# Optimization experiments

Hardware: AMD Instinct MI355X
Metric: run time of the kernel (lower is better)

The kernel has to match this reference:

```python
import jax, jax.numpy as jnp
import numpy as np

NUM_CLASSES = 21
THRESH = 0.5
VAR = (0.1, 0.2)
B, P, O = 128, 8732, 16

def setup_inputs() -> dict:
    key = jax.random.key(0)
    ks = jax.random.split(key, 7)
    loc_preds = jax.random.normal(ks[0], (B, P, 4), jnp.float32)
    score_preds = jax.random.normal(ks[1], (B, P, NUM_CLASSES), jnp.float32)
    # priors in center-size form (cx, cy, w, h)
    pc = jax.random.uniform(ks[2], (P, 2), minval=0.05, maxval=0.95)
    pwh = jax.random.uniform(ks[3], (P, 2), minval=0.05, maxval=0.4)
    priors = jnp.concatenate([pc, pwh], axis=1).astype(jnp.float32)
    # ground truth: valid point-form boxes + label in last column
    gc = jax.random.uniform(ks[4], (B, O, 2), minval=0.2, maxval=0.8)
    gwh = jax.random.uniform(ks[5], (B, O, 2), minval=0.05, maxval=0.3)
    boxes = jnp.concatenate([gc - gwh / 2, gc + gwh / 2], axis=-1)
    labels = jax.random.randint(ks[6], (B, O, 1), 1, NUM_CLASSES).astype(jnp.float32)
    gt_data = jnp.concatenate([boxes, labels], axis=-1).astype(jnp.float32)
    return {"loc_preds": loc_preds, "score_preds": score_preds,
            "gt_data": gt_data, "priors": priors}

def _iou(a, b):
    # a: (O,4) point form, b: (P,4) point form -> (O,P)
    lt = jnp.maximum(a[:, None, :2], b[None, :, :2])
    rb = jnp.minimum(a[:, None, 2:], b[None, :, 2:])
    wh = jnp.clip(rb - lt, 0.0)
    inter = wh[..., 0] * wh[..., 1]
    area_a = (a[:, 2] - a[:, 0]) * (a[:, 3] - a[:, 1])
    area_b = (b[:, 2] - b[:, 0]) * (b[:, 3] - b[:, 1])
    return inter / (area_a[:, None] + area_b[None, :] - inter)

def _encode(matched, priors):
    # matched: (P,4) point form; priors: (P,4) center-size form
    g_c = (matched[:, :2] + matched[:, 2:]) / 2 - priors[:, :2]
    g_c = g_c / (VAR[0] * priors[:, 2:])
    g_wh = (matched[:, 2:] - matched[:, :2]) / priors[:, 2:]
    g_wh = jnp.log(g_wh) / VAR[1]
    return jnp.concatenate([g_c, g_wh], axis=1)

def _match_one(gt_loc, gt_cls, priors_pt, priors):
    ious = _iou(gt_loc, priors_pt)                    # (O, P)
    best_prior_idx = jnp.argmax(ious, axis=1)         # (O,)
    best_truth_overlap = jnp.max(ious, axis=0)        # (P,)
    best_truth_idx = jnp.argmax(ious, axis=0)         # (P,)
    # ensure every gt's best prior is kept positive and assigned to that gt
    best_truth_overlap = best_truth_overlap.at[best_prior_idx].set(2.0)
    best_truth_idx = best_truth_idx.at[best_prior_idx].set(jnp.arange(gt_loc.shape[0]))
    matched = gt_loc[best_truth_idx]                  # (P, 4)
    conf = gt_cls[best_truth_idx]
    conf = jnp.where(best_truth_overlap < THRESH, 0.0, conf)
    return _encode(matched, priors), conf.astype(jnp.int32)

def reference(loc_preds, score_preds, gt_data, priors):
    priors_pt = jnp.concatenate([priors[:, :2] - priors[:, 2:] / 2,
                                 priors[:, :2] + priors[:, 2:] / 2], axis=1)
    gt_loc, gt_cls = gt_data[..., :4], gt_data[..., 4]
    loc_targets, score_targets = jax.vmap(
        lambda l, c: _match_one(l, c, priors_pt, priors))(gt_loc, gt_cls)
    pos = score_targets > 0                           # (B, P)
    num_matched = jnp.sum(pos).astype(jnp.float32)

    # SmoothL1 over positive boxes (sum reduction)
    d = jnp.abs(loc_preds - loc_targets)
    sl1 = jnp.where(d < 1.0, 0.5 * d * d, d - 0.5)    # (B, P, 4)
    loc_loss = jnp.sum(jnp.where(pos[..., None], sl1, 0.0))

    # per-box cross-entropy on all boxes
    lse = jax.nn.logsumexp(score_preds, axis=-1)      # (B, P)
    gathered = jnp.take_along_axis(score_preds, score_targets[..., None],
                                   axis=-1)[..., 0]
    ce = lse - gathered                               # (B, P)

    # hard negative mining via double argsort ranking
    mine = jnp.where(pos, 0.0, ce)
    idx = jnp.argsort(-mine, axis=1)
    rank = jnp.argsort(idx, axis=1)
    num_pos = jnp.sum(pos, axis=1)                    # (B,)
    total_pos = jnp.sum(num_pos)
    num_neg = jnp.minimum(3 * num_pos, P - total_pos - 1)
    neg = rank < num_neg[:, None]

    sel = pos | neg
    conf_loss = jnp.sum(jnp.where(sel, ce, 0.0))
    return loc_loss / num_matched, conf_loss / num_matched
```

## Files before the change

### kernel.cpp

```cpp
#include <hip/hip_runtime.h>
#include <cstdint>
#include <cstddef>

#define B 128
#define P 8732
#define NC 21
#define O 16
#define THRESH 0.5f
#define NB1 8
#define NBX2 6
#define BPB 1456
#define WPW 364
#define NPART (B * NBX2)
#define SLABF 1536

typedef unsigned long long u64;
typedef unsigned int u32;
typedef unsigned char u8;

__device__ __forceinline__ float iou_pt(float a0, float a1, float a2, float a3,
                                        float b0, float b1, float b2, float b3) {
    float ltx = fmaxf(a0, b0), lty = fmaxf(a1, b1);
    float rbx = fminf(a2, b2), rby = fminf(a3, b3);
    float wx = fmaxf(rbx - ltx, 0.0f), wy = fmaxf(rby - lty, 0.0f);
    float inter = wx * wy;
    float aa = (a2 - a0) * (a3 - a1);
    float ab = (b2 - b0) * (b3 - b1);
    return inter / (aa + ab - inter);
}

__global__ void __launch_bounds__(256) k_pass1(const float* __restrict__ gt,
                                               const float* __restrict__ priors,
                                               u64* __restrict__ bk,
                                               u8* __restrict__ bidx) {
    const int b = blockIdx.y;
    __shared__ float s_gt[O * 4];
    __shared__ u64 s_wk[4][O];
    const int tid = threadIdx.x;
    const int wave = tid >> 6, lane = tid & 63;
    if (tid < O * 4) {
        int o = tid >> 2, c = tid & 3;
        s_gt[tid] = gt[(b * O + o) * 5 + c];
    }
    __syncthreads();

    u64 lk[O];
#pragma unroll
    for (int o = 0; o < O; o++) lk[o] = 0ull;

    for (int p = blockIdx.x * 256 + tid; p < P; p += NB1 * 256) {
        float4 pr = reinterpret_cast<const float4*>(priors)[p];
        float b0 = pr.x - pr.z * 0.5f, b1 = pr.y - pr.w * 0.5f;
        float b2 = pr.x + pr.z * 0.5f, b3 = pr.y + pr.w * 0.5f;
        float bov = -1.0f; int bo = 0;
#pragma unroll
        for (int o = 0; o < O; o++) {
            float v = iou_pt(s_gt[o * 4 + 0], s_gt[o * 4 + 1], s_gt[o * 4 + 2], s_gt[o * 4 + 3],
                             b0, b1, b2, b3);
            u64 key = ((u64)__float_as_uint(v) << 32) | (u64)(0xFFFFFFFFu - (u32)p);
            lk[o] = (key > lk[o]) ? key : lk[o];
            if (v > bov) { bov = v; bo = o; }
        }
        bidx[(size_t)b * P + p] = (u8)(bo | ((bov >= THRESH) ? 0x80 : 0));
    }

#pragma unroll
    for (int o = 0; o < O; o++) {
        u64 k = lk[o];
#pragma unroll
        for (int off = 32; off > 0; off >>= 1) {
            u64 other = (u64)__shfl_xor((long long)k, off, 64);
            k = (other > k) ? other : k;
        }
        if (lane == 0) s_wk[wave][o] = k;
    }
    __syncthreads();
    if (tid < O) {
        u64 k = s_wk[0][tid];
#pragma unroll
        for (int w = 1; w < 4; w++) { u64 v = s_wk[w][tid]; k = (v > k) ? v : k; }
        bk[((size_t)b * O + tid) * NB1 + blockIdx.x] = k;
    }
}

__device__ __forceinline__ void stage64(const float* __restrict__ gsrc,
                                        float* lds, int nf4, int lane) {
    const char* src = (const char*)gsrc;
    char* dst = (char*)lds;
#pragma unroll
    for (int i = 0; i < 6; i++) {
        int idx = i * 64 + lane;
        if (idx >= nf4) idx = nf4 - 1;
        __builtin_amdgcn_global_load_lds(
            (const __attribute__((address_space(1))) u32*)(src + (size_t)idx * 16),
            (__attribute__((address_space(3))) u32*)(dst + i * 1024),
            16, 0, 0);
    }
}

__global__ void __launch_bounds__(256) k_pass2(const float* __restrict__ gt,
                                               const float* __restrict__ priors,
                                               const u64* __restrict__ bk,
                                               const u8* __restrict__ bidx,
                                               const float* __restrict__ loc_preds,
                                               const float* __restrict__ scores,
                                               float* __restrict__ mine,
                                               double* __restrict__ pl,
                                               double* __restrict__ pc,
                                               int* __restrict__ pn) {
    const int b = blockIdx.y;
    const int tid = threadIdx.x;
    const int wave = tid >> 6, lane = tid & 63;
    __shared__ float s_slab[4][2][SLABF];
    __shared__ float s_gt[O * 5];
    __shared__ int s_bp[O];

    if (tid < O * 5) s_gt[tid] = gt[b * O * 5 + tid];
    if (tid < O) {
        u64 k = bk[((size_t)b * O + tid) * NB1];
#pragma unroll
        for (int i = 1; i < NB1; i++) {
            u64 v = bk[((size_t)b * O + tid) * NB1 + i];
            k = (v > k) ? v : k;
        }
        s_bp[tid] = (int)(0xFFFFFFFFu - (u32)(k & 0xFFFFFFFFull));
    }
    __syncthreads();

    const int wbase = blockIdx.x * BPB + wave * WPW;
    int wp = P - wbase; if (wp > WPW) wp = WPW;
    const int nchunk = (wp > 0) ? ((wp + 63) >> 6) : 0;

    double l_loc = 0.0, l_ce = 0.0;
    int l_np = 0;

    if (nchunk > 0) {
        {
            int nv0 = wp < 64 ? wp : 64;
            stage64(scores + ((size_t)b * P + wbase) * NC,
                    &s_slab[wave][0][0], nv0 * 21 / 4, lane);
        }
        for (int c = 0; c < nchunk; ++c) {
            const int base = wbase + c * 64;
            int nv = wp - c * 64; if (nv > 64) nv = 64;

            if (c + 1 < nchunk) {
                int nv2 = wp - (c + 1) * 64; if (nv2 > 64) nv2 = 64;
                asm volatile("s_waitcnt lgkmcnt(0)" ::: "memory");
                stage64(scores + ((size_t)b * P + base + 64) * NC,
                        &s_slab[wave][(c + 1) & 1][0], nv2 * 21 / 4, lane);
                asm volatile("s_waitcnt vmcnt(6)" ::: "memory");
            } else {
                asm volatile("s_waitcnt vmcnt(0)" ::: "memory");
            }
            __builtin_amdgcn_sched_barrier(0);

            if (lane < nv) {
                const int p = base + lane;
                const float* fsl = &s_slab[wave][c & 1][lane * NC];
                float fs[NC];
#pragma unroll
                for (int cc = 0; cc < NC; cc++) fs[cc] = fsl[cc];

                int e = (int)bidx[(size_t)b * P + p];
                int best_idx = e & 0x3F;
                bool matched = (e & 0x80) != 0;
#pragma unroll
                for (int o = 0; o < O; o++) {
                    if (s_bp[o] == p) { best_idx = o; matched = true; }
                }
                int cls = matched ? (int)s_gt[best_idx * 5 + 4] : 0;

                float mx = fs[0];
#pragma unroll
                for (int cc = 1; cc < NC; cc++) mx = fmaxf(mx, fs[cc]);
                float se = 0.0f;
#pragma unroll
                for (int cc = 0; cc < NC; cc++) se += __expf(fs[cc] - mx);
                float lse = mx + __logf(se);
                float g = fs[0];
#pragma unroll
                for (int cc = 1; cc < NC; cc++) g = (cc == cls) ? fs[cc] : g;
                float ce = lse - g;

                bool pos = cls > 0;
                mine[(size_t)b * P + p] = pos ? 0.0f : ce;

                if (pos) {
                    l_np++;
                    l_ce += (double)ce;
                    float4 pr = reinterpret_cast<const float4*>(priors)[p];
                    float m0 = s_gt[best_idx * 5 + 0], m1 = s_gt[best_idx * 5 + 1];
                    float m2 = s_gt[best_idx * 5 + 2], m3 = s_gt[best_idx * 5 + 3];
                    float tx = ((m0 + m2) * 0.5f - pr.x) / (0.1f * pr.z);
                    float ty = ((m1 + m3) * 0.5f - pr.y) / (0.1f * pr.w);
                    float tw = __logf((m2 - m0) / pr.z) * 5.0f;
                    float th = __logf((m3 - m1) / pr.w) * 5.0f;
                    float4 lp = reinterpret_cast<const float4*>(loc_preds)[(size_t)b * P + p];
                    float d0 = fabsf(lp.x - tx), d1 = fabsf(lp.y - ty);
                    float d2 = fabsf(lp.z - tw), d3 = fabsf(lp.w - th);
                    float s0 = d0 < 1.0f ? 0.5f * d0 * d0 : d0 - 0.5f;
                    float s1 = d1 < 1.0f ? 0.5f * d1 * d1 : d1 - 0.5f;
                    float s2 = d2 < 1.0f ? 0.5f * d2 * d2 : d2 - 0.5f;
                    float s3 = d3 < 1.0f ? 0.5f * d3 * d3 : d3 - 0.5f;
                    l_loc += (double)((s0 + s1) + (s2 + s3));
                }
            }
        }
    }

#pragma unroll
    for (int off = 32; off > 0; off >>= 1) {
        l_loc += __shfl_xor(l_loc, off, 64);
        l_ce  += __shfl_xor(l_ce, off, 64);
        l_np  += __shfl_xor(l_np, off, 64);
    }
    __shared__ double s_loc[4], s_ce[4];
    __shared__ int s_np[4];
    if (lane == 0) { s_loc[wave] = l_loc; s_ce[wave] = l_ce; s_np[wave] = l_np; }
    __syncthreads();
    if (tid == 0) {
        int q = b * NBX2 + blockIdx.x;
        pl[q] = (s_loc[0] + s_loc[1]) + (s_loc[2] + s_loc[3]);
        pc[q] = (s_ce[0] + s_ce[1]) + (s_ce[2] + s_ce[3]);
        pn[q] = s_np[0] + s_np[1] + s_np[2] + s_np[3];
    }
}

__global__ void __launch_bounds__(1024) k_hardneg(const float* __restrict__ mine,
                                                  const int* __restrict__ pn,
                                                  double* __restrict__ pneg) {
    const int b = blockIdx.x;
    const int tid = threadIdx.x;
    const int lane = tid & 63, wave = tid >> 6;
    __shared__ float s_mine[P];
    __shared__ u32 s_hist[256];
    __shared__ u32 s_sel[2];
    __shared__ double s_red[16];
    __shared__ int s_ti[16];
    __shared__ int s_npx[NBX2];
    __shared__ int s_k;

    {
        int t = 0;
        for (int i = tid; i < NPART; i += 1024) t += pn[i];
#pragma unroll
        for (int off = 32; off > 0; off >>= 1) t += __shfl_xor(t, off, 64);
        if (lane == 0) s_ti[wave] = t;
    }
    if (tid < NBX2) s_npx[tid] = pn[b * NBX2 + tid];
    __syncthreads();
    if (tid == 0) {
        int tp = 0;
#pragma unroll
        for (int w = 0; w < 16; w++) tp += s_ti[w];
        int np = 0;
#pragma unroll
        for (int x = 0; x < NBX2; x++) np += s_npx[x];
        int k = 3 * np;
        int cap = P - tp - 1;
        if (cap < k) k = cap;
        s_k = k;
    }
    __syncthreads();
    const int k = s_k;

    if (k <= 0) {
        if (tid == 0) pneg[b] = 0.0;
        return;
    }

    for (int i = tid; i < P; i += 1024) s_mine[i] = mine[(size_t)b * P + i];
    if (tid == 0) { s_sel[0] = 0u; s_sel[1] = (u32)k; }
    __syncthreads();

    for (int shift = 24; shift >= 0; shift -= 8) {
        if (tid < 256) s_hist[tid] = 0u;
        __syncthreads();
        u32 prefix = s_sel[0];
        u32 kr = s_sel[1];
        u32 himask = (shift == 24) ? 0u : (0xFFFFFFFFu << (shift + 8));
        for (int i = tid; i < P; i += 1024) {
            u32 v = __float_as_uint(s_mine[i]);
            if ((v & himask) == prefix) atomicAdd(&s_hist[(v >> shift) & 255u], 1u);
        }
        __syncthreads();
        if (tid < 64) {
            const int L = tid;
            const int btop = 255 - 4 * L;
            u32 h0 = s_hist[btop], h1 = s_hist[btop - 1], h2 = s_hist[btop - 2], h3 = s_hist[btop - 3];
            u32 g4 = h0 + h1 + h2 + h3;
            u32 x = g4;
#pragma unroll
            for (int off = 1; off < 64; off <<= 1) {
                u32 v = __shfl_up(x, off, 64);
                if (L >= off) x += v;
            }
            u32 excl = x - g4;
            if (excl < kr && excl + g4 >= kr) {
                u32 c = excl; int chosen = btop; u32 kloc = kr;
                u32 nc;
                nc = c + h0; if (c < kr && nc >= kr) { chosen = btop;     kloc = kr - c; } c = nc;
                nc = c + h1; if (c < kr && nc >= kr) { chosen = btop - 1; kloc = kr - c; } c = nc;
                nc = c + h2; if (c < kr && nc >= kr) { chosen = btop - 2; kloc = kr - c; } c = nc;
                nc = c + h3; if (c < kr && nc >= kr) { chosen = btop - 3; kloc = kr - c; } c = nc;
                s_sel[0] = prefix | ((u32)chosen << shift);
                s_sel[1] = kloc;
            }
        }
        __syncthreads();
    }

    u32 tbits = s_sel[0];
    u32 kr = s_sel[1];
    float T = __uint_as_float(tbits);

    double sd = 0.0;
    for (int i = tid; i < P; i += 1024) {
        u32 v = __float_as_uint(s_mine[i]);
        if (v > tbits) sd += (double)s_mine[i];
    }
#pragma unroll
    for (int off = 32; off > 0; off >>= 1) sd += __shfl_xor(sd, off, 64);
    if (lane == 0) s_red[wave] = sd;
    __syncthreads();
    if (tid == 0) {
        double tt = 0.0;
#pragma unroll
        for (int w = 0; w < 16; w++) tt += s_red[w];
        pneg[b] = tt + (double)kr * (double)T;
    }
}

__global__ void __launch_bounds__(1024) k_fin(const double* __restrict__ pl,
                                              const double* __restrict__ pc,
                                              const int* __restrict__ pn,
                                              const double* __restrict__ pneg,
                                              float* __restrict__ out) {
    const int tid = threadIdx.x;
    const int lane = tid & 63, wave = tid >> 6;
    __shared__ double s_l[16], s_c[16], s_g[16];
    __shared__ int s_t[16];

    double tl = 0.0, tc = 0.0, tg = 0.0;
    int tn = 0;
    for (int i = tid; i < NPART; i += 1024) { tl += pl[i]; tc += pc[i]; tn += pn[i]; }
    if (tid < B) tg = pneg[tid];
#pragma unroll
    for (int off = 32; off > 0; off >>= 1) {
        tl += __shfl_xor(tl, off, 64);
        tc += __shfl_xor(tc, off, 64);
        tg += __shfl_xor(tg, off, 64);
        tn += __shfl_xor(tn, off, 64);
    }
    if (lane == 0) { s_l[wave] = tl; s_c[wave] = tc; s_g[wave] = tg; s_t[wave] = tn; }
    __syncthreads();
    if (tid == 0) {
        double al = 0.0, ac = 0.0, ag = 0.0;
        int an = 0;
#pragma unroll
        for (int w = 0; w < 16; w++) { al += s_l[w]; ac += s_c[w]; ag += s_g[w]; an += s_t[w]; }
        double n = (double)an;
        out[0] = (float)(al / n);
        out[1] = (float)((ac + ag) / n);
    }
}

extern "C" void kernel_launch(void* const* d_in, const int* in_sizes, int n_in,
                              void* d_out, int out_size, void* d_ws, size_t ws_size,
                              hipStream_t stream) {
    const float* loc_preds = (const float*)d_in[0];
    const float* scores    = (const float*)d_in[1];
    const float* gt        = (const float*)d_in[2];
    const float* priors    = (const float*)d_in[3];

    char* ws = (char*)d_ws;
    u64* bk      = (u64*)ws;
    double* pl   = (double*)(ws + 131072);
    double* pc   = (double*)(ws + 137216);
    int* pn      = (int*)(ws + 143360);
    double* pneg = (double*)(ws + 146432);
    u8* bidx     = (u8*)(ws + 147456);
    float* mine  = (float*)(ws + 1265152);


    k_pass1<<<dim3(NB1, B), dim3(256), 0, stream>>>(gt, priors, bk, bidx);
    k_pass2<<<dim3(NBX2, B), dim3(256), 0, stream>>>(
        gt, priors, bk, bidx, loc_preds, scores, mine, pl, pc, pn);
    k_hardneg<<<dim3(B), dim3(1024), 0, stream>>>(mine, pn, pneg);
    k_fin<<<dim3(1), dim3(1024), 0, stream>>>(pl, pc, pn, pneg, (float*)d_out);
}
```

Measured before the change: 58.27 us.

## Split per-prior softmax across lane pairs and double pass2 grid

Pass2 now has each pair of lanes share one prior, each lane covering about half of the 21 class scores, with the max, exp-sum and gathered logit combined via shfl_xor. Chunks drop to 32 priors, the grid doubles to 12 blocks per batch, and the LDS slab halves, all aimed at more parallelism and shorter per-thread dependency chains. Per-lane accumulators switch from double to float. The costs are extra shuffles, half the lanes idle in the positive-box tail, and slightly lower accumulation precision.

```diff
diff --git a/kernel.cpp b/kernel.cpp
--- a/kernel.cpp
+++ b/kernel.cpp
@@ -8,11 +8,11 @@
 #define O 16
 #define THRESH 0.5f
 #define NB1 8
-#define NBX2 6
-#define BPB 1456
-#define WPW 364
+#define NBX2 12
+#define BPB 736
+#define WPW 184
 #define NPART (B * NBX2)
-#define SLABF 1536
+#define SLABF 768
 
 typedef unsigned long long u64;
 typedef unsigned int u32;
@@ -83,12 +83,12 @@
     }
 }
 
-__device__ __forceinline__ void stage64(const float* __restrict__ gsrc,
+__device__ __forceinline__ void stage32(const float* __restrict__ gsrc,
                                         float* lds, int nf4, int lane) {
     const char* src = (const char*)gsrc;
     char* dst = (char*)lds;
 #pragma unroll
-    for (int i = 0; i < 6; i++) {
+    for (int i = 0; i < 3; i++) {
         int idx = i * 64 + lane;
         if (idx >= nf4) idx = nf4 - 1;
         __builtin_amdgcn_global_load_lds(
@@ -111,6 +111,7 @@
     const int b = blockIdx.y;
     const int tid = threadIdx.x;
     const int wave = tid >> 6, lane = tid & 63;
+    const int half = lane & 1;
     __shared__ float s_slab[4][2][SLABF];
     __shared__ float s_gt[O * 5];
     __shared__ int s_bp[O];
@@ -129,38 +130,40 @@
 
     const int wbase = blockIdx.x * BPB + wave * WPW;
     int wp = P - wbase; if (wp > WPW) wp = WPW;
-    const int nchunk = (wp > 0) ? ((wp + 63) >> 6) : 0;
-
-    double l_loc = 0.0, l_ce = 0.0;
+    const int nchunk = (wp > 0) ? ((wp + 31) >> 5) : 0;
+
+    float l_loc = 0.f, l_ce = 0.f;
     int l_np = 0;
 
     if (nchunk > 0) {
         {
-            int nv0 = wp < 64 ? wp : 64;
-            stage64(scores + ((size_t)b * P + wbase) * NC,
+            int nv0 = wp < 32 ? wp : 32;
+            stage32(scores + ((size_t)b * P + wbase) * NC,
                     &s_slab[wave][0][0], nv0 * 21 / 4, lane);
         }
         for (int c = 0; c < nchunk; ++c) {
-            const int base = wbase + c * 64;
-            int nv = wp - c * 64; if (nv > 64) nv = 64;
+            const int base = wbase + c * 32;
+            int nv = wp - c * 32; if (nv > 32) nv = 32;
 
             if (c + 1 < nchunk) {
-                int nv2 = wp - (c + 1) * 64; if (nv2 > 64) nv2 = 64;
+                int nv2 = wp - (c + 1) * 32; if (nv2 > 32) nv2 = 32;
                 asm volatile("s_waitcnt lgkmcnt(0)" ::: "memory");
-                stage64(scores + ((size_t)b * P + base + 64) * NC,
+                stage32(scores + ((size_t)b * P + base + 32) * NC,
                         &s_slab[wave][(c + 1) & 1][0], nv2 * 21 / 4, lane);
-                asm volatile("s_waitcnt vmcnt(6)" ::: "memory");
+                asm volatile("s_waitcnt vmcnt(3)" ::: "memory");
             } else {
                 asm volatile("s_waitcnt vmcnt(0)" ::: "memory");
             }
             __builtin_amdgcn_sched_barrier(0);
 
-            if (lane < nv) {
-                const int p = base + lane;
-                const float* fsl = &s_slab[wave][c & 1][lane * NC];
-                float fs[NC];
-#pragma unroll
-                for (int cc = 0; cc < NC; cc++) fs[cc] = fsl[cc];
+            const int pi = lane >> 1;
+            if (pi < nv) {
+                const int p = base + pi;
+                const float* sl = &s_slab[wave][c & 1][pi * NC + 11 * half];
+                float v[11];
+#pragma unroll
+                for (int i = 0; i < 11; i++) v[i] = sl[i];
+                const bool last_ok = (half == 0);
 
                 int e = (int)bidx[(size_t)b * P + p];
                 int best_idx = e & 0x3F;
@@ -171,39 +174,49 @@
                 }
                 int cls = matched ? (int)s_gt[best_idx * 5 + 4] : 0;
 
-                float mx = fs[0];
-#pragma unroll
-                for (int cc = 1; cc < NC; cc++) mx = fmaxf(mx, fs[cc]);
-                float se = 0.0f;
-#pragma unroll
-                for (int cc = 0; cc < NC; cc++) se += __expf(fs[cc] - mx);
-                float lse = mx + __logf(se);
-                float g = fs[0];
-#pragma unroll
-                for (int cc = 1; cc < NC; cc++) g = (cc == cls) ? fs[cc] : g;
+                float pm = v[0];
+#pragma unroll
+                for (int i = 1; i < 10; i++) pm = fmaxf(pm, v[i]);
+                pm = fmaxf(pm, last_ok ? v[10] : -1e30f);
+                float m = fmaxf(pm, __shfl_xor(pm, 1, 64));
+
+                float ps = 0.f;
+#pragma unroll
+                for (int i = 0; i < 10; i++) ps += __expf(v[i] - m);
+                ps += last_ok ? __expf(v[10] - m) : 0.f;
+                float tot = ps + __shfl_xor(ps, 1, 64);
+                float lse = m + __logf(tot);
+
+                float gp = 0.f;
+#pragma unroll
+                for (int i = 0; i < 11; i++) {
+                    int cc = 11 * half + i;
+                    gp += (cc == cls && (i < 10 || last_ok)) ? v[i] : 0.f;
+                }
+                float g = gp + __shfl_xor(gp, 1, 64);
                 float ce = lse - g;
 
-                bool pos = cls > 0;
-                mine[(size_t)b * P + p] = pos ? 0.0f : ce;
-
-                if (pos) {
-                    l_np++;
-                    l_ce += (double)ce;
-                    float4 pr = reinterpret_cast<const float4*>(priors)[p];
-                    float m0 = s_gt[best_idx * 5 + 0], m1 = s_gt[best_idx * 5 + 1];
-                    float m2 = s_gt[best_idx * 5 + 2], m3 = s_gt[best_idx * 5 + 3];
-                    float tx = ((m0 + m2) * 0.5f - pr.x) / (0.1f * pr.z);
-                    float ty = ((m1 + m3) * 0.5f - pr.y) / (0.1f * pr.w);
-                    float tw = __logf((m2 - m0) / pr.z) * 5.0f;
-                    float th = __logf((m3 - m1) / pr.w) * 5.0f;
-                    float4 lp = reinterpret_cast<const float4*>(loc_preds)[(size_t)b * P + p];
-                    float d0 = fabsf(lp.x - tx), d1 = fabsf(lp.y - ty);
-                    float d2 = fabsf(lp.z - tw), d3 = fabsf(lp.w - th);
-                    float s0 = d0 < 1.0f ? 0.5f * d0 * d0 : d0 - 0.5f;
-                    float s1 = d1 < 1.0f ? 0.5f * d1 * d1 : d1 - 0.5f;
-                    float s2 = d2 < 1.0f ? 0.5f * d2 * d2 : d2 - 0.5f;
-                    float s3 = d3 < 1.0f ? 0.5f * d3 * d3 : d3 - 0.5f;
-                    l_loc += (double)((s0 + s1) + (s2 + s3));
+                if (half == 0) {
+                    mine[(size_t)b * P + p] = matched ? 0.0f : ce;
+                    if (matched) {
+                        l_np++;
+                        l_ce += ce;
+                        float4 pr = reinterpret_cast<const float4*>(priors)[p];
+                        float m0 = s_gt[best_idx * 5 + 0], m1 = s_gt[best_idx * 5 + 1];
+                        float m2 = s_gt[best_idx * 5 + 2], m3 = s_gt[best_idx * 5 + 3];
+                        float tx = ((m0 + m2) * 0.5f - pr.x) / (0.1f * pr.z);
+                        float ty = ((m1 + m3) * 0.5f - pr.y) / (0.1f * pr.w);
+                        float tw = __logf((m2 - m0) / pr.z) * 5.0f;
+                        float th = __logf((m3 - m1) / pr.w) * 5.0f;
+                        float4 lp = reinterpret_cast<const float4*>(loc_preds)[(size_t)b * P + p];
+                        float d0 = fabsf(lp.x - tx), d1 = fabsf(lp.y - ty);
+                        float d2 = fabsf(lp.z - tw), d3 = fabsf(lp.w - th);
+                        float s0 = d0 < 1.0f ? 0.5f * d0 * d0 : d0 - 0.5f;
+                        float s1 = d1 < 1.0f ? 0.5f * d1 * d1 : d1 - 0.5f;
+                        float s2 = d2 < 1.0f ? 0.5f * d2 * d2 : d2 - 0.5f;
+                        float s3 = d3 < 1.0f ? 0.5f * d3 * d3 : d3 - 0.5f;
+                        l_loc += (s0 + s1) + (s2 + s3);
+                    }
                 }
             }
         }
@@ -217,7 +230,7 @@
     }
     __shared__ double s_loc[4], s_ce[4];
     __shared__ int s_np[4];
-    if (lane == 0) { s_loc[wave] = l_loc; s_ce[wave] = l_ce; s_np[wave] = l_np; }
+    if (lane == 0) { s_loc[wave] = (double)l_loc; s_ce[wave] = (double)l_ce; s_np[wave] = l_np; }
     __syncthreads();
     if (tid == 0) {
         int q = b * NBX2 + blockIdx.x;
@@ -377,11 +390,11 @@
     char* ws = (char*)d_ws;
     u64* bk      = (u64*)ws;
     double* pl   = (double*)(ws + 131072);
-    double* pc   = (double*)(ws + 137216);
-    int* pn      = (int*)(ws + 143360);
-    double* pneg = (double*)(ws + 146432);
-    u8* bidx     = (u8*)(ws + 147456);
-    float* mine  = (float*)(ws + 1265152);
+    double* pc   = (double*)(ws + 143360);
+    int* pn      = (int*)(ws + 155648);
+    double* pneg = (double*)(ws + 161792);
+    u8* bidx     = (u8*)(ws + 162816);
+    float* mine  = (float*)(ws + 1280512);
 
 
     k_pass1<<<dim3(NB1, B), dim3(256), 0, stream>>>(gt, priors, bk, bidx);
```

After: 62.38 us. +7.1%, slower.

## Triple-buffer score staging in pass2, fewer blocks, float accumulators

Applied to the files above, without the earlier changes.

Pass2 now runs four blocks per batch row instead of six, so each wave handles more priors. Score staging into LDS moves from double to triple buffering, keeping two chunks in flight with matching vmcnt waits, and the refill is issued after compute. Per-lane accumulators switch from double to float and are widened only at the wave reduction, which cuts FP64 work but can lose some precision. The positive test now uses the matched flag instead of cls>0, the workspace offsets are repacked, and the larger LDS footprint may reduce occupancy.

```diff
diff --git a/kernel.cpp b/kernel.cpp
--- a/kernel.cpp
+++ b/kernel.cpp
@@ -8,9 +8,9 @@
 #define O 16
 #define THRESH 0.5f
 #define NB1 8
-#define NBX2 6
-#define BPB 1456
-#define WPW 364
+#define NBX2 4
+#define BPB 2304
+#define WPW 576
 #define NPART (B * NBX2)
 #define SLABF 1536
 
@@ -111,7 +111,7 @@
     const int b = blockIdx.y;
     const int tid = threadIdx.x;
     const int wave = tid >> 6, lane = tid & 63;
-    __shared__ float s_slab[4][2][SLABF];
+    __shared__ float s_slab[4][3][SLABF];
     __shared__ float s_gt[O * 5];
     __shared__ int s_bp[O];
 
@@ -131,33 +131,28 @@
     int wp = P - wbase; if (wp > WPW) wp = WPW;
     const int nchunk = (wp > 0) ? ((wp + 63) >> 6) : 0;
 
-    double l_loc = 0.0, l_ce = 0.0;
+    float l_loc = 0.f, l_ce = 0.f;
     int l_np = 0;
 
     if (nchunk > 0) {
-        {
-            int nv0 = wp < 64 ? wp : 64;
-            stage64(scores + ((size_t)b * P + wbase) * NC,
-                    &s_slab[wave][0][0], nv0 * 21 / 4, lane);
+        for (int c0 = 0; c0 < 3 && c0 < nchunk; ++c0) {
+            int nv0 = wp - c0 * 64; if (nv0 > 64) nv0 = 64;
+            stage64(scores + ((size_t)b * P + wbase + c0 * 64) * NC,
+                    &s_slab[wave][c0][0], nv0 * 21 / 4, lane);
         }
         for (int c = 0; c < nchunk; ++c) {
             const int base = wbase + c * 64;
             int nv = wp - c * 64; if (nv > 64) nv = 64;
 
-            if (c + 1 < nchunk) {
-                int nv2 = wp - (c + 1) * 64; if (nv2 > 64) nv2 = 64;
-                asm volatile("s_waitcnt lgkmcnt(0)" ::: "memory");
-                stage64(scores + ((size_t)b * P + base + 64) * NC,
-                        &s_slab[wave][(c + 1) & 1][0], nv2 * 21 / 4, lane);
-                asm volatile("s_waitcnt vmcnt(6)" ::: "memory");
-            } else {
-                asm volatile("s_waitcnt vmcnt(0)" ::: "memory");
-            }
+            int ahead = nchunk - 1 - c; if (ahead > 2) ahead = 2;
+            if (ahead == 2)      asm volatile("s_waitcnt vmcnt(12)" ::: "memory");
+            else if (ahead == 1) asm volatile("s_waitcnt vmcnt(6)" ::: "memory");
+            else                 asm volatile("s_waitcnt vmcnt(0)" ::: "memory");
             __builtin_amdgcn_sched_barrier(0);
 
             if (lane < nv) {
                 const int p = base + lane;
-                const float* fsl = &s_slab[wave][c & 1][lane * NC];
+                const float* fsl = &s_slab[wave][c % 3][lane * NC];
                 float fs[NC];
 #pragma unroll
                 for (int cc = 0; cc < NC; cc++) fs[cc] = fsl[cc];
@@ -183,12 +178,11 @@
                 for (int cc = 1; cc < NC; cc++) g = (cc == cls) ? fs[cc] : g;
                 float ce = lse - g;
 
-                bool pos = cls > 0;
-                mine[(size_t)b * P + p] = pos ? 0.0f : ce;
-
-                if (pos) {
+                mine[(size_t)b * P + p] = matched ? 0.0f : ce;
+
+                if (matched) {
                     l_np++;
-                    l_ce += (double)ce;
+                    l_ce += ce;
                     float4 pr = reinterpret_cast<const float4*>(priors)[p];
                     float m0 = s_gt[best_idx * 5 + 0], m1 = s_gt[best_idx * 5 + 1];
                     float m2 = s_gt[best_idx * 5 + 2], m3 = s_gt[best_idx * 5 + 3];
@@ -203,8 +197,15 @@
                     float s1 = d1 < 1.0f ? 0.5f * d1 * d1 : d1 - 0.5f;
                     float s2 = d2 < 1.0f ? 0.5f * d2 * d2 : d2 - 0.5f;
                     float s3 = d3 < 1.0f ? 0.5f * d3 * d3 : d3 - 0.5f;
-                    l_loc += (double)((s0 + s1) + (s2 + s3));
+                    l_loc += (s0 + s1) + (s2 + s3);
                 }
+            }
+
+            if (c + 3 < nchunk) {
+                int nv3 = wp - (c + 3) * 64; if (nv3 > 64) nv3 = 64;
+                asm volatile("s_waitcnt lgkmcnt(0)" ::: "memory");
+                stage64(scores + ((size_t)b * P + base + 3 * 64) * NC,
+                        &s_slab[wave][c % 3][0], nv3 * 21 / 4, lane);
             }
         }
     }
@@ -217,7 +218,7 @@
     }
     __shared__ double s_loc[4], s_ce[4];
     __shared__ int s_np[4];
-    if (lane == 0) { s_loc[wave] = l_loc; s_ce[wave] = l_ce; s_np[wave] = l_np; }
+    if (lane == 0) { s_loc[wave] = (double)l_loc; s_ce[wave] = (double)l_ce; s_np[wave] = l_np; }
     __syncthreads();
     if (tid == 0) {
         int q = b * NBX2 + blockIdx.x;
@@ -377,11 +378,11 @@
     char* ws = (char*)d_ws;
     u64* bk      = (u64*)ws;
     double* pl   = (double*)(ws + 131072);
-    double* pc   = (double*)(ws + 137216);
-    int* pn      = (int*)(ws + 143360);
-    double* pneg = (double*)(ws + 146432);
-    u8* bidx     = (u8*)(ws + 147456);
-    float* mine  = (float*)(ws + 1265152);
+    double* pc   = (double*)(ws + 135168);
+    int* pn      = (int*)(ws + 139264);
+    double* pneg = (double*)(ws + 141312);
+    u8* bidx     = (u8*)(ws + 142336);
+    float* mine  = (float*)(ws + 1260032);
 
 
     k_pass1<<<dim3(NB1, B), dim3(256), 0, stream>>>(gt, priors, bk, bidx);
```

Measured after the change: 60.99 us. 4.7% more time.

## Fold final reduction into hard-negative kernel via atomic ticket and float accumulators

Applied to the files above, without the earlier changes.

Removes the separate single-block finalize kernel. Each hard-negative block atomically adds its negative sum to a global double, and the last block to take a ticket reduces the partials and writes the output. Per-thread loss accumulation in pass2 switches from double to float, and the positive test uses the matched flag instead of the class. This saves one kernel launch and some FP64 work, at the cost of float rounding in the partial sums and a global-atomic ordering dependency.

```diff
diff --git a/kernel.cpp b/kernel.cpp
--- a/kernel.cpp
+++ b/kernel.cpp
@@ -32,12 +32,15 @@
 __global__ void __launch_bounds__(256) k_pass1(const float* __restrict__ gt,
                                                const float* __restrict__ priors,
                                                u64* __restrict__ bk,
-                                               u8* __restrict__ bidx) {
+                                               u8* __restrict__ bidx,
+                                               double* __restrict__ acc,
+                                               u32* __restrict__ ticket) {
     const int b = blockIdx.y;
     __shared__ float s_gt[O * 4];
     __shared__ u64 s_wk[4][O];
     const int tid = threadIdx.x;
     const int wave = tid >> 6, lane = tid & 63;
+    if (blockIdx.x == 0 && b == 0 && tid == 0) { acc[0] = 0.0; *ticket = 0u; }
     if (tid < O * 4) {
         int o = tid >> 2, c = tid & 3;
         s_gt[tid] = gt[(b * O + o) * 5 + c];
@@ -131,7 +134,7 @@
     int wp = P - wbase; if (wp > WPW) wp = WPW;
     const int nchunk = (wp > 0) ? ((wp + 63) >> 6) : 0;
 
-    double l_loc = 0.0, l_ce = 0.0;
+    float l_loc = 0.f, l_ce = 0.f;
     int l_np = 0;
 
     if (nchunk > 0) {
@@ -183,12 +186,11 @@
                 for (int cc = 1; cc < NC; cc++) g = (cc == cls) ? fs[cc] : g;
                 float ce = lse - g;
 
-                bool pos = cls > 0;
-                mine[(size_t)b * P + p] = pos ? 0.0f : ce;
-
-                if (pos) {
+                mine[(size_t)b * P + p] = matched ? 0.0f : ce;
+
+                if (matched) {
                     l_np++;
-                    l_ce += (double)ce;
+                    l_ce += ce;
                     float4 pr = reinterpret_cast<const float4*>(priors)[p];
                     float m0 = s_gt[best_idx * 5 + 0], m1 = s_gt[best_idx * 5 + 1];
                     float m2 = s_gt[best_idx * 5 + 2], m3 = s_gt[best_idx * 5 + 3];
@@ -203,7 +205,7 @@
                     float s1 = d1 < 1.0f ? 0.5f * d1 * d1 : d1 - 0.5f;
                     float s2 = d2 < 1.0f ? 0.5f * d2 * d2 : d2 - 0.5f;
                     float s3 = d3 < 1.0f ? 0.5f * d3 * d3 : d3 - 0.5f;
-                    l_loc += (double)((s0 + s1) + (s2 + s3));
+                    l_loc += (s0 + s1) + (s2 + s3);
                 }
             }
         }
@@ -217,7 +219,7 @@
     }
     __shared__ double s_loc[4], s_ce[4];
     __shared__ int s_np[4];
-    if (lane == 0) { s_loc[wave] = l_loc; s_ce[wave] = l_ce; s_np[wave] = l_np; }
+    if (lane == 0) { s_loc[wave] = (double)l_loc; s_ce[wave] = (double)l_ce; s_np[wave] = l_np; }
     __syncthreads();
     if (tid == 0) {
         int q = b * NBX2 + blockIdx.x;
@@ -228,8 +230,12 @@
 }
 
 __global__ void __launch_bounds__(1024) k_hardneg(const float* __restrict__ mine,
+                                                  const double* __restrict__ pl,
+                                                  const double* __restrict__ pc,
                                                   const int* __restrict__ pn,
-                                                  double* __restrict__ pneg) {
+                                                  double* __restrict__ acc,
+                                                  u32* __restrict__ ticket,
+                                                  float* __restrict__ out) {
     const int b = blockIdx.x;
     const int tid = threadIdx.x;
     const int lane = tid & 63, wave = tid >> 6;
@@ -239,7 +245,7 @@
     __shared__ double s_red[16];
     __shared__ int s_ti[16];
     __shared__ int s_npx[NBX2];
-    __shared__ int s_k;
+    __shared__ int s_k, s_tp;
 
     {
         int t = 0;
@@ -261,108 +267,100 @@
         int cap = P - tp - 1;
         if (cap < k) k = cap;
         s_k = k;
+        s_tp = tp;
     }
     __syncthreads();
     const int k = s_k;
 
-    if (k <= 0) {
-        if (tid == 0) pneg[b] = 0.0;
-        return;
-    }
-
-    for (int i = tid; i < P; i += 1024) s_mine[i] = mine[(size_t)b * P + i];
-    if (tid == 0) { s_sel[0] = 0u; s_sel[1] = (u32)k; }
-    __syncthreads();
-
-    for (int shift = 24; shift >= 0; shift -= 8) {
-        if (tid < 256) s_hist[tid] = 0u;
+    if (k > 0) {
+        for (int i = tid; i < P; i += 1024) s_mine[i] = mine[(size_t)b * P + i];
+        if (tid == 0) { s_sel[0] = 0u; s_sel[1] = (u32)k; }
         __syncthreads();
-        u32 prefix = s_sel[0];
+
+        for (int shift = 24; shift >= 0; shift -= 8) {
+            if (tid < 256) s_hist[tid] = 0u;
+            __syncthreads();
+            u32 prefix = s_sel[0];
+            u32 kr = s_sel[1];
+            u32 himask = (shift == 24) ? 0u : (0xFFFFFFFFu << (shift + 8));
+            for (int i = tid; i < P; i += 1024) {
+                u32 v = __float_as_uint(s_mine[i]);
+                if ((v & himask) == prefix) atomicAdd(&s_hist[(v >> shift) & 255u], 1u);
+            }
+            __syncthreads();
+            if (tid < 64) {
+                const int L = tid;
+                const int btop = 255 - 4 * L;
+                u32 h0 = s_hist[btop], h1 = s_hist[btop - 1], h2 = s_hist[btop - 2], h3 = s_hist[btop - 3];
+                u32 g4 = h0 + h1 + h2 + h3;
+                u32 x = g4;
+#pragma unroll
+                for (int off = 1; off < 64; off <<= 1) {
+                    u32 v = __shfl_up(x, off, 64);
+                    if (L >= off) x += v;
+                }
+                u32 excl = x - g4;
+                if (excl < kr && excl + g4 >= kr) {
+                    u32 c = excl; int chosen = btop; u32 kloc = kr;
+                    u32 nc;
+                    nc = c + h0; if (c < kr && nc >= kr) { chosen = btop;     kloc = kr - c; } c = nc;
+                    nc = c + h1; if (c < kr && nc >= kr) { chosen = btop - 1; kloc = kr - c; } c = nc;
+                    nc = c + h2; if (c < kr && nc >= kr) { chosen = btop - 2; kloc = kr - c; } c = nc;
+                    nc = c + h3; if (c < kr && nc >= kr) { chosen = btop - 3; kloc = kr - c; } c = nc;
+                    s_sel[0] = prefix | ((u32)chosen << shift);
+                    s_sel[1] = kloc;
+                }
+            }
+            __syncthreads();
+        }
+
+        u32 tbits = s_sel[0];
         u32 kr = s_sel[1];
-        u32 himask = (shift == 24) ? 0u : (0xFFFFFFFFu << (shift + 8));
+        float T = __uint_as_float(tbits);
+
+        double sd = 0.0;
         for (int i = tid; i < P; i += 1024) {
             u32 v = __float_as_uint(s_mine[i]);
-            if ((v & himask) == prefix) atomicAdd(&s_hist[(v >> shift) & 255u], 1u);
-        }
+            if (v > tbits) sd += (double)s_mine[i];
+        }
+#pragma unroll
+        for (int off = 32; off > 0; off >>= 1) sd += __shfl_xor(sd, off, 64);
+        if (lane == 0) s_red[wave] = sd;
         __syncthreads();
-        if (tid < 64) {
-            const int L = tid;
-            const int btop = 255 - 4 * L;
-            u32 h0 = s_hist[btop], h1 = s_hist[btop - 1], h2 = s_hist[btop - 2], h3 = s_hist[btop - 3];
-            u32 g4 = h0 + h1 + h2 + h3;
-            u32 x = g4;
-#pragma unroll
-            for (int off = 1; off < 64; off <<= 1) {
-                u32 v = __shfl_up(x, off, 64);
-                if (L >= off) x += v;
-            }
-            u32 excl = x - g4;
-            if (excl < kr && excl + g4 >= kr) {
-                u32 c = excl; int chosen = btop; u32 kloc = kr;
-                u32 nc;
-                nc = c + h0; if (c < kr && nc >= kr) { chosen = btop;     kloc = kr - c; } c = nc;
-                nc = c + h1; if (c < kr && nc >= kr) { chosen = btop - 1; kloc = kr - c; } c = nc;
-                nc = c + h2; if (c < kr && nc >= kr) { chosen = btop - 2; kloc = kr - c; } c = nc;
-                nc = c + h3; if (c < kr && nc >= kr) { chosen = btop - 3; kloc = kr - c; } c = nc;
-                s_sel[0] = prefix | ((u32)chosen << shift);
-                s_sel[1] = kloc;
-            }
-        }
+        if (tid == 0) {
+            double tt = 0.0;
+#pragma unroll
+            for (int w = 0; w < 16; w++) tt += s_red[w];
+            atomicAdd(&acc[0], tt + (double)kr * (double)T);
+        }
+    }
+
+    __threadfence();
+    __syncthreads();
+    __shared__ int s_last;
+    if (tid == 0) s_last = (atomicAdd(ticket, 1u) == B - 1) ? 1 : 0;
+    __syncthreads();
+    if (s_last) {
+        __shared__ double f_l[16], f_c[16];
+        double tl = 0.0, tc = 0.0;
+        for (int i = tid; i < NPART; i += 1024) { tl += pl[i]; tc += pc[i]; }
+#pragma unroll
+        for (int off = 32; off > 0; off >>= 1) {
+            tl += __shfl_xor(tl, off, 64);
+            tc += __shfl_xor(tc, off, 64);
+        }
+        if (lane == 0) { f_l[wave] = tl; f_c[wave] = tc; }
         __syncthreads();
-    }
-
-    u32 tbits = s_sel[0];
-    u32 kr = s_sel[1];
-    float T = __uint_as_float(tbits);
-
-    double sd = 0.0;
-    for (int i = tid; i < P; i += 1024) {
-        u32 v = __float_as_uint(s_mine[i]);
-        if (v > tbits) sd += (double)s_mine[i];
-    }
-#pragma unroll
-    for (int off = 32; off > 0; off >>= 1) sd += __shfl_xor(sd, off, 64);
-    if (lane == 0) s_red[wave] = sd;
-    __syncthreads();
-    if (tid == 0) {
-        double tt = 0.0;
-#pragma unroll
-        for (int w = 0; w < 16; w++) tt += s_red[w];
-        pneg[b] = tt + (double)kr * (double)T;
-    }
-}
-
-__global__ void __launch_bounds__(1024) k_fin(const double* __restrict__ pl,
-                                              const double* __restrict__ pc,
-                                              const int* __restrict__ pn,
-                                              const double* __restrict__ pneg,
-                                              float* __restrict__ out) {
-    const int tid = threadIdx.x;
-    const int lane = tid & 63, wave = tid >> 6;
-    __shared__ double s_l[16], s_c[16], s_g[16];
-    __shared__ int s_t[16];
-
-    double tl = 0.0, tc = 0.0, tg = 0.0;
-    int tn = 0;
-    for (int i = tid; i < NPART; i += 1024) { tl += pl[i]; tc += pc[i]; tn += pn[i]; }
-    if (tid < B) tg = pneg[tid];
-#pragma unroll
-    for (int off = 32; off > 0; off >>= 1) {
-        tl += __shfl_xor(tl, off, 64);
-        tc += __shfl_xor(tc, off, 64);
-        tg += __shfl_xor(tg, off, 64);
-        tn += __shfl_xor(tn, off, 64);
-    }
-    if (lane == 0) { s_l[wave] = tl; s_c[wave] = tc; s_g[wave] = tg; s_t[wave] = tn; }
-    __syncthreads();
-    if (tid == 0) {
-        double al = 0.0, ac = 0.0, ag = 0.0;
-        int an = 0;
-#pragma unroll
-        for (int w = 0; w < 16; w++) { al += s_l[w]; ac += s_c[w]; ag += s_g[w]; an += s_t[w]; }
-        double n = (double)an;
-        out[0] = (float)(al / n);
-        out[1] = (float)((ac + ag) / n);
+        if (tid == 0) {
+            double al = 0.0, ac = 0.0;
+#pragma unroll
+            for (int w = 0; w < 16; w++) { al += f_l[w]; ac += f_c[w]; }
+            __threadfence();
+            double ag = atomicAdd(&acc[0], 0.0);
+            double n = (double)s_tp;
+            out[0] = (float)(al / n);
+            out[1] = (float)((ac + ag) / n);
+        }
     }
 }
 
@@ -379,14 +377,15 @@
     double* pl   = (double*)(ws + 131072);
     double* pc   = (double*)(ws + 137216);
     int* pn      = (int*)(ws + 143360);
-    double* pneg = (double*)(ws + 146432);
-    u8* bidx     = (u8*)(ws + 147456);
-    float* mine  = (float*)(ws + 1265152);
-
-
-    k_pass1<<<dim3(NB1, B), dim3(256), 0, stream>>>(gt, priors, bk, bidx);
+    double* acc  = (double*)(ws + 146432);
+    u32* ticket  = (u32*)(ws + 146440);
+    u8* bidx     = (u8*)(ws + 146448);
+    float* mine  = (float*)(ws + 1264160);
+
+
+    k_pass1<<<dim3(NB1, B), dim3(256), 0, stream>>>(gt, priors, bk, bidx, acc, ticket);
     k_pass2<<<dim3(NBX2, B), dim3(256), 0, stream>>>(
         gt, priors, bk, bidx, loc_preds, scores, mine, pl, pc, pn);
-    k_hardneg<<<dim3(B), dim3(1024), 0, stream>>>(mine, pn, pneg);
-    k_fin<<<dim3(1), dim3(1024), 0, stream>>>(pl, pc, pn, pneg, (float*)d_out);
-}
+    k_hardneg<<<dim3(B), dim3(1024), 0, stream>>>(mine, pl, pc, pn, acc, ticket,
+                                                  (float*)d_out);
+}
```

After: 86.02 us. +47.6%, slower.
